# Performance work log

Measured on AMD Instinct MI355X. Metric: run time of the kernel, lower is better.

Reference implementation:

```python
import jax, jax.numpy as jnp
import numpy as np

SIGMA = 4.0
RADIUS = int(4.0 * SIGMA + 0.5)  # scipy gaussian_filter truncate=4.0 -> radius 16


def _gaussian_kernel():
    x = jnp.arange(-RADIUS, RADIUS + 1, dtype=jnp.float32)
    k = jnp.exp(-0.5 * (x / SIGMA) ** 2)
    return k / k.sum()


def _blur_last_axis(x):
    # separable 1D gaussian along last axis with reflect padding (scipy default mode)
    k = _gaussian_kernel()
    pad = [(0, 0)] * (x.ndim - 1) + [(RADIUS, RADIUS)]
    xp = jnp.pad(x, pad, mode='reflect')
    xr = xp.reshape(-1, 1, xp.shape[-1])  # [N, C=1, L]
    out = jax.lax.conv_general_dilated(xr, k.reshape(1, 1, -1), (1,), 'VALID')
    return out.reshape(x.shape)


def _gaussian_blur2d(img):
    # img: [B, H, W]
    img = _blur_last_axis(img)                       # blur W
    img = jnp.swapaxes(_blur_last_axis(jnp.swapaxes(img, -1, -2)), -1, -2)  # blur H
    return img


def setup_inputs() -> dict:
    key = jax.random.key(0)
    k1, k2 = jax.random.split(key)
    M, Q, D = 50000, 3136, 1024
    return {
        'coreset': jax.random.normal(k1, (M, D), dtype=jnp.float32),
        'features': jax.random.normal(k2, (Q, D), dtype=jnp.float32),
        'batchsize': 4,
        'grid_h': 28,
        'grid_w': 28,
        'out_h': 224,
        'out_w': 224,
    }


def reference(coreset, features, batchsize, grid_h, grid_w, out_h, out_w):
    # _compute_batchwise_differences: sqrt(clamp(|a|^2 - 2ab + |b|^2, 0))
    a2 = jnp.sum(coreset * coreset, axis=-1, keepdims=True)      # [M, 1]
    b2 = jnp.sum(features * features, axis=-1)[None, :]           # [1, Q]
    ab = jnp.einsum('md,qd->mq', coreset, features)               # [M, Q]
    dists = jnp.sqrt(jnp.clip(a2 - 2.0 * ab + b2, 0.0, None))     # [M, Q]
    patch_scores = dists.min(axis=0)                              # [Q] = min(0).values

    # unpatch_scores + PatchMaker.score (max over patches)
    per_image = patch_scores.reshape(batchsize, -1)               # [B, P]
    image_scores = per_image.max(axis=-1)                         # [B]

    # RescaleSegmentor.convert_to_segmentation: bilinear upsample + gaussian blur
    grid = patch_scores.reshape(batchsize, grid_h, grid_w)        # [B, Hp, Wp]
    masks = jax.image.resize(grid, (batchsize, out_h, out_w), method='bilinear')
    masks = _gaussian_blur2d(masks)                               # sigma=4 smoothing
    return image_scores, masks
```

## Files before the change

### kernel.cpp

```cpp
#include <hip/hip_runtime.h>


typedef unsigned short ushort_t;
typedef unsigned int uint32;
typedef __bf16 bf16x8 __attribute__((ext_vector_type(8)));
typedef float f32x4 __attribute__((ext_vector_type(4)));

#define M_ROWS 50000
#define M_PAD  50048
#define M_TILES 391
#define Q_ROWS 3136
#define Q_PAD  3200
#define Q_TILES 25
#define DDIM   1024
#define NKT    (DDIM / 64)
#define FLT_BIG 3.402823466e+38f

typedef __attribute__((address_space(1))) const void* as1_cvoid;
typedef __attribute__((address_space(3))) void* as3_void;

__device__ __forceinline__ void load16_lds(const void* g, void* l) {
  __builtin_amdgcn_global_load_lds((as1_cvoid)g, (as3_void)l, 16, 0, 0);
}

__device__ __forceinline__ ushort_t f2bf(float f) {
  uint32 u = __float_as_uint(f);
  u += 0x7FFFu + ((u >> 16) & 1u);
  return (ushort_t)(u >> 16);
}
__device__ __forceinline__ uint32 f2key(float f) {
  uint32 b = __float_as_uint(f);
  return (b & 0x80000000u) ? ~b : (b | 0x80000000u);
}
__device__ __forceinline__ float key2f(uint32 k) {
  uint32 b = (k & 0x80000000u) ? (k ^ 0x80000000u) : ~k;
  return __uint_as_float(b);
}

__global__ void k_init(uint32* __restrict__ mk) {
  int i = blockIdx.x * 256 + threadIdx.x;
  if (i < Q_PAD) mk[i] = 0xFFFFFFFFu;
}

__global__ void k_convert(const float* __restrict__ src, ushort_t* __restrict__ dst,
                          float* __restrict__ norm, int valid_rows, float pad_norm) {
  const int row = blockIdx.x * 4 + (threadIdx.x >> 6);
  const int lane = threadIdx.x & 63;
  if (row < valid_rows) {
    const float4* s = (const float4*)(src + (size_t)row * DDIM);
    ushort4* d = (ushort4*)(dst + (size_t)row * DDIM);
    float ss = 0.f;
    #pragma unroll
    for (int u = 0; u < 4; ++u) {
      const float4 v = s[lane + 64 * u];
      ss += v.x * v.x + v.y * v.y + v.z * v.z + v.w * v.w;
      ushort4 o;
      o.x = f2bf(v.x); o.y = f2bf(v.y); o.z = f2bf(v.z); o.w = f2bf(v.w);
      d[lane + 64 * u] = o;
    }
    #pragma unroll
    for (int off = 32; off; off >>= 1) ss += __shfl_xor(ss, off);
    if (lane == 0) norm[row] = ss;
  } else {
    ushort4 z; z.x = z.y = z.z = z.w = 0;
    ushort4* d = (ushort4*)(dst + (size_t)row * DDIM);
    #pragma unroll
    for (int u = 0; u < 4; ++u) d[lane + 64 * u] = z;
    if (lane == 0) norm[row] = pad_norm;
  }
}

__global__ __launch_bounds__(256) void k_gemm_min(
    const ushort_t* __restrict__ A,
    const ushort_t* __restrict__ B,
    const float* __restrict__ a2, const float* __restrict__ b2,
    uint32* __restrict__ mk) {
  __shared__ __align__(16) ushort_t As[2][128 * 64];
  __shared__ __align__(16) ushort_t Bs[2][128 * 64];
  __shared__ float a2s[128];
  __shared__ float red[2][64];

  const int tid = threadIdx.x;
  const int lane = tid & 63;
  const int wid = tid >> 6;
  const int wr = wid >> 1;
  const int wc = wid & 1;

  const int nwg = M_TILES * Q_TILES;
  const int q8 = nwg >> 3, r8 = nwg & 7;
  const int w = blockIdx.x;
  const int xcd = w & 7, idx = w >> 3;
  const int nw = (xcd < r8 ? xcd * (q8 + 1) : r8 * (q8 + 1) + (xcd - r8) * q8) + idx;
  const int mt = nw / Q_TILES;
  const int qt = nw - mt * Q_TILES;
  const int m0 = mt * 128;
  const int q0 = qt * 128;

  if (tid < 128) a2s[tid] = a2[m0 + tid];

  f32x4 acc[4][4];
  #pragma unroll
  for (int i = 0; i < 4; ++i)
    #pragma unroll
    for (int j = 0; j < 4; ++j)
      #pragma unroll
      for (int e = 0; e < 4; ++e) acc[i][j][e] = 0.f;

  const int kb = lane >> 4;
  const int col = lane & 15;
  const int swz = col & 7;
  const int srow = tid >> 3;
  const int scb = tid & 7;
  const int ssw = scb ^ (srow & 7);

  #define STAGE(p, kbase_)                                                   \
    {                                                                        \
      _Pragma("unroll")                                                      \
      for (int it = 0; it < 4; ++it) {                                       \
        const int row_ = it * 32 + srow;                                     \
        load16_lds(A + (size_t)(m0 + row_) * DDIM + (kbase_) + ssw * 8,      \
                   &As[p][it * 2048 + wid * 512]);                           \
        load16_lds(B + (size_t)(q0 + row_) * DDIM + (kbase_) + ssw * 8,      \
                   &Bs[p][it * 2048 + wid * 512]);                           \
      }                                                                      \
    }

  STAGE(0, 0)
  __syncthreads();

  for (int kt = 0; kt < NKT; ++kt) {
    const int cur = kt & 1;
    if (kt + 1 < NKT) STAGE(cur ^ 1, (kt + 1) * 64)
    #pragma unroll
    for (int kk = 0; kk < 2; ++kk) {
      bf16x8 af[4], bfr[4];
      #pragma unroll
      for (int i = 0; i < 4; ++i)
        af[i] = *reinterpret_cast<const bf16x8*>(
            &As[cur][(wr * 64 + i * 16 + col) * 64 + ((kk * 4 + kb) ^ swz) * 8]);
      #pragma unroll
      for (int j = 0; j < 4; ++j)
        bfr[j] = *reinterpret_cast<const bf16x8*>(
            &Bs[cur][(wc * 64 + j * 16 + col) * 64 + ((kk * 4 + kb) ^ swz) * 8]);
      #pragma unroll
      for (int i = 0; i < 4; ++i)
        #pragma unroll
        for (int j = 0; j < 4; ++j)
          acc[i][j] = __builtin_amdgcn_mfma_f32_16x16x32_bf16(af[i], bfr[j],
                                                              acc[i][j], 0, 0, 0);
    }
    __syncthreads();
  }

  float v[4];
  #pragma unroll
  for (int j = 0; j < 4; ++j) {
    float mn = FLT_BIG;
    #pragma unroll
    for (int i = 0; i < 4; ++i)
      #pragma unroll
      for (int r = 0; r < 4; ++r) {
        const int ml = wr * 64 + i * 16 + kb * 4 + r;
        mn = fminf(mn, a2s[ml] - 2.0f * acc[i][j][r]);
      }
    mn = fminf(mn, __shfl_xor(mn, 16));
    mn = fminf(mn, __shfl_xor(mn, 32));
    v[j] = mn;
  }
  if (wr == 1 && lane < 16) {
    #pragma unroll
    for (int j = 0; j < 4; ++j) red[wc][j * 16 + lane] = v[j];
  }
  __syncthreads();
  if (wr == 0 && lane < 16) {
    #pragma unroll
    for (int j = 0; j < 4; ++j) {
      const int q = q0 + wc * 64 + j * 16 + lane;
      const float s = fminf(v[j], red[wc][j * 16 + lane]) + b2[q];
      atomicMin(&mk[q], f2key(s));
    }
  }
}

__global__ void k_finalize(const uint32* __restrict__ mk, float* __restrict__ ps,
                           float* __restrict__ out_scores) {
  const int b = blockIdx.x;
  const int tid = threadIdx.x;
  float vmax = -FLT_BIG;
  for (int t = tid; t < 784; t += 256) {
    const int q = b * 784 + t;
    float s = fmaxf(key2f(mk[q]), 0.f);
    const float p = sqrtf(s);
    ps[q] = p;
    vmax = fmaxf(vmax, p);
  }
  #pragma unroll
  for (int off = 32; off; off >>= 1) vmax = fmaxf(vmax, __shfl_xor(vmax, off));
  __shared__ float wm[4];
  if ((tid & 63) == 0) wm[tid >> 6] = vmax;
  __syncthreads();
  if (tid == 0) out_scores[b] = fmaxf(fmaxf(wm[0], wm[1]), fmaxf(wm[2], wm[3]));
}

__device__ __forceinline__ int reflect224(int i) {
  if (i < 0) i = -i;
  if (i > 223) i = 446 - i;
  return i;
}

__global__ void k_mkC(float* __restrict__ C) {
  const int idx = blockIdx.x * 256 + threadIdx.x;
  if (idx >= 224 * 28) return;
  const int o = idx / 28;
  const int g = idx - o * 28;
  float acc = 0.f, wsum = 0.f;
  for (int t = 0; t < 33; ++t) {
    const float d = (float)(t - 16);
    const float wb = expf(-0.03125f * d * d);
    wsum += wb;
    const int y = reflect224(o + t - 16);
    float fy = ((float)y + 0.5f) * 0.125f - 0.5f;
    int iy = (int)floorf(fy);
    float wy = fy - (float)iy;
    if (iy < 0)   { iy = 0;  wy = 0.f; }
    if (iy >= 27) { iy = 27; wy = 0.f; }
    const int iy1 = min(iy + 1, 27);
    float bw = 0.f;
    if (g == iy)  bw += 1.f - wy;
    if (g == iy1) bw += wy;
    acc += wb * bw;
  }
  C[idx] = acc / wsum;
}

__global__ void k_mask1(const float* __restrict__ ps, const float* __restrict__ C,
                        float* __restrict__ T) {
  const int idx = blockIdx.x * 256 + threadIdx.x;
  if (idx >= 4 * 28 * 224) return;
  const int X = idx % 224;
  const int gy = (idx / 224) % 28;
  const int b = idx / (224 * 28);
  const float* Crow = C + X * 28;
  const float* prow = ps + (b * 28 + gy) * 28;
  float s = 0.f;
  #pragma unroll
  for (int gx = 0; gx < 28; ++gx) s += Crow[gx] * prow[gx];
  T[idx] = s;
}

__global__ void k_mask2(const float* __restrict__ T, const float* __restrict__ C,
                        float* __restrict__ out) {
  const int idx = blockIdx.x * 256 + threadIdx.x;
  if (idx >= 4 * 224 * 224) return;
  const int X = idx % 224;
  const int Y = (idx / 224) % 224;
  const int b = idx / (224 * 224);
  const float* Crow = C + Y * 28;
  float s = 0.f;
  #pragma unroll
  for (int gy = 0; gy < 28; ++gy) s += Crow[gy] * T[(b * 28 + gy) * 224 + X];
  out[idx] = s;
}

extern "C" void kernel_launch(void* const* d_in, const int* in_sizes, int n_in,
                              void* d_out, int out_size, void* d_ws, size_t ws_size,
                              hipStream_t stream) {
  const float* cs = (const float*)d_in[0];
  const float* ft = (const float*)d_in[1];
  float* out = (float*)d_out;

  const size_t OFF_FT = (size_t)M_PAD * DDIM * 2;
  const size_t OFF_A2 = OFF_FT + (size_t)Q_PAD * DDIM * 2;
  const size_t OFF_B2 = OFF_A2 + (size_t)M_PAD * 4;
  const size_t OFF_MK = OFF_B2 + (size_t)Q_PAD * 4;
  const size_t OFF_PS = OFF_MK + (size_t)Q_PAD * 4;
  const size_t OFF_C  = OFF_PS + (size_t)Q_ROWS * 4;
  const size_t OFF_T  = OFF_C + (size_t)224 * 28 * 4;

  char* ws = (char*)d_ws;
  ushort_t* csb = (ushort_t*)(ws);
  ushort_t* ftb = (ushort_t*)(ws + OFF_FT);
  float* a2 = (float*)(ws + OFF_A2);
  float* b2 = (float*)(ws + OFF_B2);
  uint32* mk = (uint32*)(ws + OFF_MK);
  float* ps = (float*)(ws + OFF_PS);
  float* C  = (float*)(ws + OFF_C);
  float* T  = (float*)(ws + OFF_T);

  k_init<<<(Q_PAD + 255) / 256, 256, 0, stream>>>(mk);
  k_convert<<<M_PAD / 4, 256, 0, stream>>>(cs, csb, a2, M_ROWS, FLT_BIG);
  k_convert<<<Q_PAD / 4, 256, 0, stream>>>(ft, ftb, b2, Q_ROWS, 0.f);
  k_gemm_min<<<M_TILES * Q_TILES, 256, 0, stream>>>(csb, ftb, a2, b2, mk);
  k_finalize<<<4, 256, 0, stream>>>(mk, ps, out);
  k_mkC<<<(224 * 28 + 255) / 256, 256, 0, stream>>>(C);
  k_mask1<<<(4 * 28 * 224 + 255) / 256, 256, 0, stream>>>(ps, C, T);
  k_mask2<<<(4 * 224 * 224 + 255) / 256, 256, 0, stream>>>(T, C, out + 4);
}
```

Baseline: 761.8 us.

## Enlarge GEMM-min tiles to 256x256 with 8 waves and interleaved staging

The distance GEMM moves from 128x128 tiles with 4 waves to 256x256 tiles with 8 waves, each wave holding an 8x4 block of MFMA accumulators. This halves the global-to-LDS traffic per FLOP and cuts the number of workgroups and atomicMin calls. The K loop is rewritten as a hand-scheduled pipeline: global_load_lds stages for later k-tiles are issued in quarter-tile chunks between MFMA groups, with explicit vmcnt/lgkmcnt waits, barriers and s_setprio around the MFMA bursts. In exchange the kernel needs 128KB of LDS per block, so only one block fits per CU, and the padding overhead on M and Q grows.

```diff
diff --git a/kernel.cpp b/kernel.cpp
--- a/kernel.cpp
+++ b/kernel.cpp
@@ -7,13 +7,13 @@
 typedef float f32x4 __attribute__((ext_vector_type(4)));
 
 #define M_ROWS 50000
-#define M_PAD  50048
-#define M_TILES 391
+#define M_PAD  50176
+#define M_TILES 196
 #define Q_ROWS 3136
-#define Q_PAD  3200
-#define Q_TILES 25
+#define Q_PAD  3328
+#define Q_TILES 13
 #define DDIM   1024
-#define NKT    (DDIM / 64)
+#define NKT    16
 #define FLT_BIG 3.402823466e+38f
 
 typedef __attribute__((address_space(1))) const void* as1_cvoid;
@@ -36,6 +36,12 @@
   uint32 b = (k & 0x80000000u) ? (k ^ 0x80000000u) : ~k;
   return __uint_as_float(b);
 }
+
+#define WAITVM6 asm volatile("s_waitcnt vmcnt(6)" ::: "memory")
+#define WAITVM0 asm volatile("s_waitcnt vmcnt(0)" ::: "memory")
+#define WAITVM8 asm volatile("s_waitcnt vmcnt(8)" ::: "memory")
+#define LGKM0   asm volatile("s_waitcnt lgkmcnt(0)" ::: "memory")
+#define BAR()   __builtin_amdgcn_s_barrier()
 
 __global__ void k_init(uint32* __restrict__ mk) {
   int i = blockIdx.x * 256 + threadIdx.x;
@@ -70,21 +76,21 @@
   }
 }
 
-__global__ __launch_bounds__(256) void k_gemm_min(
+__global__ __launch_bounds__(512, 2) void k_gemm_min(
     const ushort_t* __restrict__ A,
     const ushort_t* __restrict__ B,
     const float* __restrict__ a2, const float* __restrict__ b2,
     uint32* __restrict__ mk) {
-  __shared__ __align__(16) ushort_t As[2][128 * 64];
-  __shared__ __align__(16) ushort_t Bs[2][128 * 64];
-  __shared__ float a2s[128];
-  __shared__ float red[2][64];
+  __shared__ __align__(16) ushort_t As[2][256 * 64];
+  __shared__ __align__(16) ushort_t Bs[2][256 * 64];
+  __shared__ float a2s[256];
+  __shared__ float red[4][64];
 
   const int tid = threadIdx.x;
   const int lane = tid & 63;
   const int wid = tid >> 6;
-  const int wr = wid >> 1;
-  const int wc = wid & 1;
+  const int wr = wid >> 2;
+  const int wc = wid & 3;
 
   const int nwg = M_TILES * Q_TILES;
   const int q8 = nwg >> 3, r8 = nwg & 7;
@@ -93,14 +99,14 @@
   const int nw = (xcd < r8 ? xcd * (q8 + 1) : r8 * (q8 + 1) + (xcd - r8) * q8) + idx;
   const int mt = nw / Q_TILES;
   const int qt = nw - mt * Q_TILES;
-  const int m0 = mt * 128;
-  const int q0 = qt * 128;
-
-  if (tid < 128) a2s[tid] = a2[m0 + tid];
-
-  f32x4 acc[4][4];
-  #pragma unroll
-  for (int i = 0; i < 4; ++i)
+  const int m0 = mt * 256;
+  const int q0 = qt * 256;
+
+  if (tid < 256) a2s[tid] = a2[m0 + tid];
+
+  f32x4 acc[8][4];
+  #pragma unroll
+  for (int i = 0; i < 8; ++i)
     #pragma unroll
     for (int j = 0; j < 4; ++j)
       #pragma unroll
@@ -109,47 +115,96 @@
   const int kb = lane >> 4;
   const int col = lane & 15;
   const int swz = col & 7;
-  const int srow = tid >> 3;
-  const int scb = tid & 7;
-  const int ssw = scb ^ (srow & 7);
-
-  #define STAGE(p, kbase_)                                                   \
-    {                                                                        \
-      _Pragma("unroll")                                                      \
-      for (int it = 0; it < 4; ++it) {                                       \
-        const int row_ = it * 32 + srow;                                     \
-        load16_lds(A + (size_t)(m0 + row_) * DDIM + (kbase_) + ssw * 8,      \
-                   &As[p][it * 2048 + wid * 512]);                           \
-        load16_lds(B + (size_t)(q0 + row_) * DDIM + (kbase_) + ssw * 8,      \
-                   &Bs[p][it * 2048 + wid * 512]);                           \
-      }                                                                      \
-    }
-
-  STAGE(0, 0)
-  __syncthreads();
-
-  for (int kt = 0; kt < NKT; ++kt) {
-    const int cur = kt & 1;
-    if (kt + 1 < NKT) STAGE(cur ^ 1, (kt + 1) * 64)
-    #pragma unroll
-    for (int kk = 0; kk < 2; ++kk) {
-      bf16x8 af[4], bfr[4];
-      #pragma unroll
-      for (int i = 0; i < 4; ++i)
-        af[i] = *reinterpret_cast<const bf16x8*>(
-            &As[cur][(wr * 64 + i * 16 + col) * 64 + ((kk * 4 + kb) ^ swz) * 8]);
-      #pragma unroll
-      for (int j = 0; j < 4; ++j)
-        bfr[j] = *reinterpret_cast<const bf16x8*>(
-            &Bs[cur][(wc * 64 + j * 16 + col) * 64 + ((kk * 4 + kb) ^ swz) * 8]);
-      #pragma unroll
-      for (int i = 0; i < 4; ++i)
-        #pragma unroll
-        for (int j = 0; j < 4; ++j)
-          acc[i][j] = __builtin_amdgcn_mfma_f32_16x16x32_bf16(af[i], bfr[j],
-                                                              acc[i][j], 0, 0, 0);
-    }
-    __syncthreads();
+
+  const int swc = (tid & 7) ^ ((tid >> 3) & 7);
+  const ushort_t* Abase = A + (size_t)(m0 + (tid >> 3)) * DDIM + swc * 8;
+  const ushort_t* Bbase = B + (size_t)(q0 + (tid >> 3)) * DDIM + swc * 8;
+  const int ldsoff = wid * 512;
+
+  #define STG_A(bufi, row0, v) \
+    load16_lds(Abase + (size_t)(row0) * DDIM + (v) * 64, &As[bufi][(row0) * 64] + ldsoff)
+  #define STG_B(bufi, row0, v) \
+    load16_lds(Bbase + (size_t)(row0) * DDIM + (v) * 64, &Bs[bufi][(row0) * 64] + ldsoff)
+
+  #define LDA(row, kk) (*reinterpret_cast<const bf16x8*>( \
+      &As[buf][(row) * 64 + ((((kk) * 4 + kb) ^ swz) << 3)]))
+  #define LDB(row, kk) (*reinterpret_cast<const bf16x8*>( \
+      &Bs[buf][(row) * 64 + ((((kk) * 4 + kb) ^ swz) << 3)]))
+
+  STG_B(0, 0, 0);   STG_B(0, 64, 0);  STG_B(0, 128, 0); STG_B(0, 192, 0);
+  STG_A(0, 0, 0);   STG_A(0, 128, 0); STG_A(0, 64, 0);  STG_A(0, 192, 0);
+  STG_B(1, 0, 1);   STG_B(1, 64, 1);  STG_B(1, 128, 1); STG_B(1, 192, 1);
+  STG_A(1, 0, 1);   STG_A(1, 128, 1); STG_A(1, 64, 1);  STG_A(1, 192, 1);
+  WAITVM8;
+  BAR();
+
+  #define MFMA_ROW(q_)                                                        \
+    _Pragma("unroll")                                                         \
+    for (int m = 0; m < 2; ++m)                                               \
+      _Pragma("unroll")                                                       \
+      for (int n = 0; n < 4; ++n)                                             \
+        _Pragma("unroll")                                                     \
+        for (int kk = 0; kk < 2; ++kk)                                        \
+          acc[(q_) * 2 + m][n] = __builtin_amdgcn_mfma_f32_16x16x32_bf16(     \
+              af[m][kk], bff[n][kk], acc[(q_) * 2 + m][n], 0, 0, 0);
+
+  #define KTILE(t, bufp_)                                                     \
+  {                                                                           \
+    const int buf = (bufp_);                                                  \
+    bf16x8 bff[4][2], af[2][2];                                               \
+                               \
+    _Pragma("unroll")                                                         \
+    for (int n = 0; n < 4; ++n)                                               \
+      _Pragma("unroll")                                                       \
+      for (int kk = 0; kk < 2; ++kk) bff[n][kk] = LDB(wc * 64 + n * 16 + col, kk); \
+    _Pragma("unroll")                                                         \
+    for (int m = 0; m < 2; ++m)                                               \
+      _Pragma("unroll")                                                       \
+      for (int kk = 0; kk < 2; ++kk) af[m][kk] = LDA(wr * 128 + m * 16 + col, kk); \
+    if ((t) >= 1 && (t) <= NKT - 2) {                                         \
+      STG_A(buf ^ 1, 64, (t) + 1); STG_A(buf ^ 1, 192, (t) + 1);              \
+    }                                                                         \
+    BAR(); LGKM0;                                                             \
+    __builtin_amdgcn_s_setprio(1); MFMA_ROW(0); __builtin_amdgcn_s_setprio(0);\
+    BAR();                                                                    \
+                                       \
+    _Pragma("unroll")                                                         \
+    for (int m = 0; m < 2; ++m)                                               \
+      _Pragma("unroll")                                                       \
+      for (int kk = 0; kk < 2; ++kk)                                          \
+        af[m][kk] = LDA(wr * 128 + 32 + m * 16 + col, kk);                    \
+    if ((t) <= NKT - 3) { STG_B(buf, 0, (t) + 2); STG_B(buf, 64, (t) + 2); }  \
+    BAR(); LGKM0;                                                             \
+    __builtin_amdgcn_s_setprio(1); MFMA_ROW(1); __builtin_amdgcn_s_setprio(0);\
+    BAR();                                                                    \
+                                       \
+    _Pragma("unroll")                                                         \
+    for (int m = 0; m < 2; ++m)                                               \
+      _Pragma("unroll")                                                       \
+      for (int kk = 0; kk < 2; ++kk)                                          \
+        af[m][kk] = LDA(wr * 128 + 64 + m * 16 + col, kk);                    \
+    if ((t) <= NKT - 3) { STG_B(buf, 128, (t) + 2); STG_B(buf, 192, (t) + 2);}\
+    BAR(); LGKM0;                                                             \
+    __builtin_amdgcn_s_setprio(1); MFMA_ROW(2); __builtin_amdgcn_s_setprio(0);\
+    BAR();                                                                    \
+            \
+    _Pragma("unroll")                                                         \
+    for (int m = 0; m < 2; ++m)                                               \
+      _Pragma("unroll")                                                       \
+      for (int kk = 0; kk < 2; ++kk)                                          \
+        af[m][kk] = LDA(wr * 128 + 96 + m * 16 + col, kk);                    \
+    if ((t) <= NKT - 3) { STG_A(buf, 0, (t) + 2); STG_A(buf, 128, (t) + 2); } \
+    BAR(); LGKM0;                                                             \
+    __builtin_amdgcn_s_setprio(1); MFMA_ROW(3); __builtin_amdgcn_s_setprio(0);\
+    if ((t) <= NKT - 3) { WAITVM6; }                                          \
+    else if ((t) == NKT - 2) { WAITVM0; }                                     \
+    BAR();                                                                    \
+  }
+
+  for (int tt = 0; tt < NKT / 2; ++tt) {
+    const int te = 2 * tt;
+    KTILE(te, 0)
+    KTILE(te + 1, 1)
   }
 
   float v[4];
@@ -157,10 +212,10 @@
   for (int j = 0; j < 4; ++j) {
     float mn = FLT_BIG;
     #pragma unroll
-    for (int i = 0; i < 4; ++i)
+    for (int i = 0; i < 8; ++i)
       #pragma unroll
       for (int r = 0; r < 4; ++r) {
-        const int ml = wr * 64 + i * 16 + kb * 4 + r;
+        const int ml = wr * 128 + i * 16 + kb * 4 + r;
         mn = fminf(mn, a2s[ml] - 2.0f * acc[i][j][r]);
       }
     mn = fminf(mn, __shfl_xor(mn, 16));
@@ -290,7 +345,7 @@
   k_init<<<(Q_PAD + 255) / 256, 256, 0, stream>>>(mk);
   k_convert<<<M_PAD / 4, 256, 0, stream>>>(cs, csb, a2, M_ROWS, FLT_BIG);
   k_convert<<<Q_PAD / 4, 256, 0, stream>>>(ft, ftb, b2, Q_ROWS, 0.f);
-  k_gemm_min<<<M_TILES * Q_TILES, 256, 0, stream>>>(csb, ftb, a2, b2, mk);
+  k_gemm_min<<<M_TILES * Q_TILES, 512, 0, stream>>>(csb, ftb, a2, b2, mk);
   k_finalize<<<4, 256, 0, stream>>>(mk, ps, out);
   k_mkC<<<(224 * 28 + 255) / 256, 256, 0, stream>>>(C);
   k_mask1<<<(4 * 28 * 224 + 255) / 256, 256, 0, stream>>>(ps, C, T);
```

Result: faster. 649.7 us (-14.7%).
